# Kernel optimization log

Measured on AMD Instinct MI355X. Metric: run time of the kernel, lower is better.

Reference implementation:

```python
import jax, jax.numpy as jnp
import numpy as np

# Geometry constants (from init_kwargs)
H = 512            # volume rows
W = 512            # volume cols
N_ANGLES = 512     # number of projections
N_DET = 736        # detector bins (covers sqrt(2)*512 ~ 724 diagonal)
N_SAMP = 736       # integration samples along each ray
DET_SPACING = 1.0
STEP = 1.0         # ray sampling step (pixel units)


def _bilinear(img, px, py):
    """Bilinear interpolation of img[H,W] at float coords (px=col, py=row); zero outside."""
    x0 = jnp.floor(px)
    y0 = jnp.floor(py)
    fx = px - x0
    fy = py - y0
    x0i = x0.astype(jnp.int32)
    y0i = y0.astype(jnp.int32)

    def tap(yi, xi):
        valid = (xi >= 0) & (xi < W) & (yi >= 0) & (yi < H)
        v = img[jnp.clip(yi, 0, H - 1), jnp.clip(xi, 0, W - 1)]
        return jnp.where(valid, v, jnp.float32(0))

    v00 = tap(y0i, x0i)
    v01 = tap(y0i, x0i + 1)
    v10 = tap(y0i + 1, x0i)
    v11 = tap(y0i + 1, x0i + 1)
    return (v00 * (1 - fx) + v01 * fx) * (1 - fy) + (v10 * (1 - fx) + v11 * fx) * fy


def _parallel_projection2d(img, angles):
    """Parallel-beam Radon transform of img[H,W] -> sinogram [A, N_DET]."""
    cx = (W - 1) * 0.5
    cy = (H - 1) * 0.5
    # detector offsets s and ray-parameter samples t, centered
    s = (jnp.arange(N_DET, dtype=jnp.float32) - (N_DET - 1) * 0.5) * DET_SPACING
    t = (jnp.arange(N_SAMP, dtype=jnp.float32) - (N_SAMP - 1) * 0.5) * STEP

    def project_angle(theta):
        c = jnp.cos(theta)
        si = jnp.sin(theta)
        # ray point = s * (c, si) + t * (-si, c), shifted to image center. [D, T]
        px = s[:, None] * c - t[None, :] * si + cx
        py = s[:, None] * si + t[None, :] * c + cy
        return _bilinear(img, px, py).sum(axis=-1) * STEP  # [D]

    # sequential map over angles keeps intermediates at [D, T] instead of [A, D, T]
    return jax.lax.map(project_angle, angles)  # [A, D]


def setup_inputs() -> dict:
    key = jax.random.key(0)
    k1, k2 = jax.random.split(key)
    x = jax.random.normal(k1, (1, H, W), dtype=jnp.float32)
    # reco variable is constrained non-negative in the original (clip_by_value(x,0,inf))
    reco = jax.random.uniform(k2, (1, H, W), dtype=jnp.float32)
    angles = jnp.linspace(0.0, np.pi, N_ANGLES, endpoint=False, dtype=jnp.float32)
    return {"x": x, "reco": reco, "angles": angles}


def reference(x, reco, angles):
    updated_reco = x + reco                               # [1, H, W]
    sino = jax.vmap(lambda im: _parallel_projection2d(im, angles))(updated_reco)  # [1, A, D]
    return sino, reco
```

## Files before the change

kernel.cpp:

```cpp
#include <hip/hip_runtime.h>
#include <hip/hip_fp16.h>
#include <climits>


namespace {
constexpr int H = 512, W = 512, NA = 512, ND = 736, NS = 736;
constexpr int SINO_SIZE = NA * ND;
constexpr int IMG_SIZE = H * W;
constexpr int QN = 514;
constexpr int QS = 520;
constexpr int QUAD_SIZE = QN * QS;
constexpr int KSPLIT = 8;
}

typedef __fp16 h2 __attribute__((ext_vector_type(2)));
typedef float  f2 __attribute__((ext_vector_type(2)));

__global__ __launch_bounds__(256) void prep_quads(const float* __restrict__ x,
                                                  const float* __restrict__ reco,
                                                  uint2* __restrict__ Q,
                                                  uint2* __restrict__ QT,
                                                  float* __restrict__ reco_out,
                                                  float* __restrict__ sino) {
    __shared__ float tile[34][35];
    const int tx = threadIdx.x, ty = threadIdx.y;
    const int r0 = blockIdx.y * 32, c0 = blockIdx.x * 32;
    const int z  = blockIdx.z;

    if (z == 0) {
        const int nthr = 289 * 256;
        const int gtid = (blockIdx.y * 17 + blockIdx.x) * 256 + ty * 32 + tx;
        for (int i = gtid; i < SINO_SIZE; i += nthr) sino[i] = 0.f;
    }

    for (int li = ty * 32 + tx; li < 34 * 34; li += 256) {
        const int yy = li / 34, xx = li - yy * 34;
        const int r = r0 - 1 + yy, c = c0 - 1 + xx;
        float v = 0.f;
        if ((unsigned)r < 512u && (unsigned)c < 512u) {
            const int i = r * W + c;
            v = x[i] + reco[i];
        }
        tile[yy][xx] = v;
    }
    __syncthreads();

    const int t2 = ty + 8 * z;
    const int ri = r0 + t2, ci = c0 + tx;
    if (ri < QN && ci < QN) {
        uint2 q;
        q.x = __builtin_bit_cast(unsigned int,
              __builtin_amdgcn_cvt_pkrtz(tile[t2][tx],     tile[t2 + 1][tx]));
        q.y = __builtin_bit_cast(unsigned int,
              __builtin_amdgcn_cvt_pkrtz(tile[t2][tx + 1], tile[t2 + 1][tx + 1]));
        Q[ri * QS + ci] = q;
    }
    const int ri2 = c0 + t2, ci2 = r0 + tx;
    if (ri2 < QN && ci2 < QN) {
        uint2 q;
        q.x = __builtin_bit_cast(unsigned int,
              __builtin_amdgcn_cvt_pkrtz(tile[tx][t2],     tile[tx][t2 + 1]));
        q.y = __builtin_bit_cast(unsigned int,
              __builtin_amdgcn_cvt_pkrtz(tile[tx + 1][t2], tile[tx + 1][t2 + 1]));
        QT[ri2 * QS + ci2] = q;
    }
    const int rr = r0 + t2, cc = c0 + tx;
    if (rr < H && cc < W) reco_out[rr * W + cc] = reco[rr * W + cc];
}

__device__ inline void range1(float p0, float inc, float lo, float hi,
                              float& klo, float& khi) {
    if (inc > 1e-6f)       { klo = (lo - p0) / inc; khi = (hi - p0) / inc; }
    else if (inc < -1e-6f) { klo = (hi - p0) / inc; khi = (lo - p0) / inc; }
    else if (p0 >= lo && p0 <= hi) { klo = -1e9f; khi = 1e9f; }
    else                   { klo = 1e9f;  khi = -1e9f; }
}

__global__ __launch_bounds__(128) void proj_quad(const uint2* __restrict__ Q,
                                                 const uint2* __restrict__ QT,
                                                 const float* __restrict__ angles,
                                                 float* __restrict__ sino) {
    const int lane = threadIdx.x & 63;
    const int d = blockIdx.x * 128 + (threadIdx.x >> 6) * 64 + lane;
    const int a = blockIdx.y;
    const int z = blockIdx.z;

    float si, co;
    sincosf(angles[a], &si, &co);

    const float cx = (W - 1) * 0.5f, cy = (H - 1) * 0.5f;
    const float s  = (float)d - (ND - 1) * 0.5f;
    const float bx = fmaf(s, co, cx);
    const float by = fmaf(s, si, cy);

    const uint2* base;
    float f0, fi, s0, sl, dS;
    if (fabsf(co) >= fabsf(si)) { base = Q;  f0 = bx; fi = -si; s0 = by; sl = co;  dS = si; }
    else                        { base = QT; f0 = by; fi = co;  s0 = bx; sl = -si; dS = co; }

    const float t0 = -(float)(NS - 1) * 0.5f;
    float F0 = fmaf(t0, fi, f0);
    float S0 = fmaf(t0, sl, s0);
    if (sl < 0.f) {
        F0 = fmaf((float)(NS - 1), fi, F0); fi = -fi;
        S0 = fmaf((float)(NS - 1), sl, S0); sl = -sl;
    }

    float kloF, khiF, kloS, khiS;
    range1(F0, fi, -0.9999f, 511.9999f, kloF, khiF);
    range1(S0, sl, -0.9999f, 511.9999f, kloS, khiS);
    const int kA = max(0,      (int)ceilf(fmaxf(kloF, kloS)));
    const int kB = min(NS - 1, (int)floorf(fminf(khiF, khiS)));

    const int o = (int)rintf(-(float)lane * dS / sl);
    const float F1 = fmaf((float)o, fi, F0) + 1.f;
    const float S1 = fmaf((float)o, sl, S0) + 1.f;

    int jA, jB;
    if (kA <= kB) { jA = kA - o; jB = kB - o; }
    else          { jA = INT_MAX; jB = INT_MIN; }
    int Jlo = jA, Jhi = jB;
    #pragma unroll
    for (int off = 1; off < 64; off <<= 1) {
        Jlo = min(Jlo, __shfl_xor(Jlo, off));
        Jhi = max(Jhi, __shfl_xor(Jhi, off));
    }
    if (Jlo > Jhi) return;
    const int L  = Jhi - Jlo + 1;
    const int js = __builtin_amdgcn_readfirstlane(Jlo + (L * z) / KSPLIT);
    const int je = __builtin_amdgcn_readfirstlane(Jlo + (L * (z + 1)) / KSPLIT - 1);
    const int n  = je - js + 1;
    const int je2 = js + 2 * (n >> 1) - 1;

    const f2 fi2 = {fi, fi}, sl2 = {sl, sl};
    const f2 F12 = {F1, F1}, S12 = {S1, S1};
    f2 jf2 = {(float)js, (float)(js + 1)};
    float acc0 = 0.f, acc1 = 0.f;
    #pragma unroll 4
    for (int j = js; j <= je2; j += 2) {
        f2 pf = jf2 * fi2 + F12;
        f2 ps = jf2 * sl2 + S12;
        jf2 += (f2)2.f;
        pf = __builtin_elementwise_min(__builtin_elementwise_max(pf, (f2)0.f), (f2)513.f);
        ps = __builtin_elementwise_min(__builtin_elementwise_max(ps, (f2)0.f), (f2)513.f);
        const f2 ff = {__builtin_floorf(pf.x), __builtin_floorf(pf.y)};
        const f2 sf = {__builtin_floorf(ps.x), __builtin_floorf(ps.y)};
        const f2 fx = pf - ff;
        const f2 fy = ps - sf;
        const f2 gy = (f2)1.f - fy;
        const f2 aif = sf * (f2)520.f + ff;
        const unsigned a0 = (unsigned)aif.x;
        const unsigned a1 = (unsigned)aif.y;
        const uint2 q0 = base[a0];
        const uint2 q1 = base[a1];
        {
            const h2 l = __builtin_bit_cast(h2, q0.x);
            const h2 r = __builtin_bit_cast(h2, q0.y);
            const h2 fxx = __builtin_amdgcn_cvt_pkrtz(fx.x, fx.x);
            const h2 m = l + fxx * (r - l);
            const h2 wy = __builtin_amdgcn_cvt_pkrtz(gy.x, fy.x);
#if __has_builtin(__builtin_amdgcn_fdot2)
            acc0 = __builtin_amdgcn_fdot2(wy, m, acc0, false);
#else
            acc0 += (float)wy.x * (float)m.x + (float)wy.y * (float)m.y;
#endif
        }
        {
            const h2 l = __builtin_bit_cast(h2, q1.x);
            const h2 r = __builtin_bit_cast(h2, q1.y);
            const h2 fxx = __builtin_amdgcn_cvt_pkrtz(fx.y, fx.y);
            const h2 m = l + fxx * (r - l);
            const h2 wy = __builtin_amdgcn_cvt_pkrtz(gy.y, fy.y);
#if __has_builtin(__builtin_amdgcn_fdot2)
            acc1 = __builtin_amdgcn_fdot2(wy, m, acc1, false);
#else
            acc1 += (float)wy.x * (float)m.x + (float)wy.y * (float)m.y;
#endif
        }
    }
    if (n & 1) {
        const float jf = (float)je;
        float pf = fmaf(jf, fi, F1);
        float ps = fmaf(jf, sl, S1);
        pf = fminf(fmaxf(pf, 0.f), 513.f);
        ps = fminf(fmaxf(ps, 0.f), 513.f);
        const float ff = floorf(pf), sf = floorf(ps);
        const float fx = pf - ff,   fy = ps - sf;
        const unsigned ai = (unsigned)fmaf(sf, 520.f, ff);
        const uint2 q = base[ai];
        const h2 l = __builtin_bit_cast(h2, q.x);
        const h2 r = __builtin_bit_cast(h2, q.y);
        const h2 fxx = __builtin_amdgcn_cvt_pkrtz(fx, fx);
        const h2 m = l + fxx * (r - l);
        const h2 wy = __builtin_amdgcn_cvt_pkrtz(1.f - fy, fy);
#if __has_builtin(__builtin_amdgcn_fdot2)
        acc0 = __builtin_amdgcn_fdot2(wy, m, acc0, false);
#else
        acc0 += (float)wy.x * (float)m.x + (float)wy.y * (float)m.y;
#endif
    }
    const float acc = acc0 + acc1;
    if (d < ND)
        __hip_atomic_fetch_add(&sino[a * ND + d], acc,
                               __ATOMIC_RELAXED, __HIP_MEMORY_SCOPE_AGENT);
}

__global__ __launch_bounds__(256) void proj_fused(const float* __restrict__ A,
                                                  const float* __restrict__ B,
                                                  const float* __restrict__ angles,
                                                  float* __restrict__ sino) {
    const int d = blockIdx.x * blockDim.x + threadIdx.x;
    const int a = blockIdx.y;
    if (d >= ND) return;
    float si, c;
    sincosf(angles[a], &si, &c);
    const float cx = (W - 1) * 0.5f, cy = (H - 1) * 0.5f;
    const float s  = (float)d - (ND - 1) * 0.5f;
    const float bx = fmaf(s, c, cx), by = fmaf(s, si, cy);
    const float t0 = -(float)(NS - 1) * 0.5f;
    float acc = 0.f;
    for (int k = 0; k < NS; ++k) {
        const float t = t0 + (float)k;
        const float px = fmaf(t, -si, bx), py = fmaf(t, c, by);
        const float x0f = floorf(px), y0f = floorf(py);
        const float fx = px - x0f, fy = py - y0f;
        const int ix = (int)x0f, iy = (int)y0f;
        auto tap = [&](int yi, int xi) -> float {
            if (xi < 0 || xi >= W || yi < 0 || yi >= H) return 0.f;
            return A[yi * W + xi] + B[yi * W + xi];
        };
        float v = 0.f;
        if (ix >= -1 && iy >= -1 && ix <= W - 1 && iy <= H - 1) {
            const float v00 = tap(iy, ix),     v01 = tap(iy, ix + 1);
            const float v10 = tap(iy + 1, ix), v11 = tap(iy + 1, ix + 1);
            const float top = fmaf(fx, v01 - v00, v00);
            const float bot = fmaf(fx, v11 - v10, v10);
            v = fmaf(fy, bot - top, top);
        }
        acc += v;
    }
    sino[a * ND + d] = acc;
}

__global__ void prep_copy(const float* __restrict__ reco, float* __restrict__ reco_out) {
    int i = blockIdx.x * blockDim.x + threadIdx.x;
    if (i < IMG_SIZE) reco_out[i] = reco[i];
}

extern "C" void kernel_launch(void* const* d_in, const int* in_sizes, int n_in,
                              void* d_out, int out_size, void* d_ws, size_t ws_size,
                              hipStream_t stream) {
    const float* x      = (const float*)d_in[0];
    const float* reco   = (const float*)d_in[1];
    const float* angles = (const float*)d_in[2];
    float* sino     = (float*)d_out;
    float* reco_out = sino + SINO_SIZE;

    const size_t need_quads = 2 * (size_t)QUAD_SIZE * sizeof(uint2);

    if (ws_size >= need_quads) {
        uint2* Q  = (uint2*)d_ws;
        uint2* QT = Q + QUAD_SIZE;
        prep_quads<<<dim3(17, 17, 4), dim3(32, 8), 0, stream>>>(x, reco, Q, QT, reco_out, sino);
        proj_quad<<<dim3(6, NA, KSPLIT), dim3(128), 0, stream>>>(Q, QT, angles, sino);
    } else {
        prep_copy<<<dim3((IMG_SIZE + 255) / 256), dim3(256), 0, stream>>>(reco, reco_out);
        proj_fused<<<dim3((ND + 255) / 256, NA), dim3(256), 0, stream>>>(x, reco, angles, sino);
    }
}
```

Measured before the change: 147.7 us.

## Store horizontal deltas in quads and split loop into clamp-free interior

The precomputed fp16 quads now hold the left value and the right-minus-left difference, so the interpolation becomes one packed fma instead of a subtract plus an fma. The sample loop is split into a wave-uniform interior range, where every lane's sample is known to be in bounds, plus scalar clamped prologue and epilogue loops. Inside the interior the per-sample min/max clamping is dropped, and the two fx conversions are packed into a single cvt. In exchange the kernel does an extra range computation and reduction, and storing differences in fp16 changes rounding slightly.

Measured after the change: 160.8 us. +8.8%, slower.

```diff
diff --git a/kernel.cpp b/kernel.cpp
--- a/kernel.cpp
+++ b/kernel.cpp
@@ -52,7 +52,8 @@
         q.x = __builtin_bit_cast(unsigned int,
               __builtin_amdgcn_cvt_pkrtz(tile[t2][tx],     tile[t2 + 1][tx]));
         q.y = __builtin_bit_cast(unsigned int,
-              __builtin_amdgcn_cvt_pkrtz(tile[t2][tx + 1], tile[t2 + 1][tx + 1]));
+              __builtin_amdgcn_cvt_pkrtz(tile[t2][tx + 1]     - tile[t2][tx],
+                                         tile[t2 + 1][tx + 1] - tile[t2 + 1][tx]));
         Q[ri * QS + ci] = q;
     }
     const int ri2 = c0 + t2, ci2 = r0 + tx;
@@ -61,7 +62,8 @@
         q.x = __builtin_bit_cast(unsigned int,
               __builtin_amdgcn_cvt_pkrtz(tile[tx][t2],     tile[tx][t2 + 1]));
         q.y = __builtin_bit_cast(unsigned int,
-              __builtin_amdgcn_cvt_pkrtz(tile[tx + 1][t2], tile[tx + 1][t2 + 1]));
+              __builtin_amdgcn_cvt_pkrtz(tile[tx + 1][t2]     - tile[tx][t2],
+                                         tile[tx + 1][t2 + 1] - tile[tx][t2 + 1]));
         QT[ri2 * QS + ci2] = q;
     }
     const int rr = r0 + t2, cc = c0 + tx;
@@ -74,6 +76,30 @@
     else if (inc < -1e-6f) { klo = (hi - p0) / inc; khi = (lo - p0) / inc; }
     else if (p0 >= lo && p0 <= hi) { klo = -1e9f; khi = 1e9f; }
     else                   { klo = 1e9f;  khi = -1e9f; }
+}
+
+__device__ __forceinline__ void samp_clamped(const uint2* __restrict__ base,
+                                             float F1, float S1, float fi, float sl,
+                                             int j, float& acc) {
+    const float jf = (float)j;
+    float pf = fmaf(jf, fi, F1);
+    float ps = fmaf(jf, sl, S1);
+    pf = fminf(fmaxf(pf, 0.f), 513.f);
+    ps = fminf(fmaxf(ps, 0.f), 513.f);
+    const float ff = floorf(pf), sf = floorf(ps);
+    const float fx = pf - ff,   fy = ps - sf;
+    const unsigned ai = (unsigned)fmaf(sf, 520.f, ff);
+    const uint2 q = base[ai];
+    const h2 l  = __builtin_bit_cast(h2, q.x);
+    const h2 dl = __builtin_bit_cast(h2, q.y);
+    const h2 fxx = __builtin_amdgcn_cvt_pkrtz(fx, fx);
+    const h2 m = fxx * dl + l;
+    const h2 wy = __builtin_amdgcn_cvt_pkrtz(1.f - fy, fy);
+#if __has_builtin(__builtin_amdgcn_fdot2)
+    acc = __builtin_amdgcn_fdot2(wy, m, acc, false);
+#else
+    acc += (float)wy.x * (float)m.x + (float)wy.y * (float)m.y;
+#endif
 }
 
 __global__ __launch_bounds__(128) void proj_quad(const uint2* __restrict__ Q,
@@ -112,93 +138,98 @@
     const int kA = max(0,      (int)ceilf(fmaxf(kloF, kloS)));
     const int kB = min(NS - 1, (int)floorf(fminf(khiF, khiS)));
 
+    float iloF, ihiF, iloS, ihiS;
+    range1(F0, fi, -0.999f, 511.999f, iloF, ihiF);
+    range1(S0, sl, -0.999f, 511.999f, iloS, ihiS);
+    const int kAI = max(0,      (int)ceilf(fmaxf(iloF, iloS)));
+    const int kBI = min(NS - 1, (int)floorf(fminf(ihiF, ihiS)));
+
     const int o = (int)rintf(-(float)lane * dS / sl);
     const float F1 = fmaf((float)o, fi, F0) + 1.f;
     const float S1 = fmaf((float)o, sl, S0) + 1.f;
 
-    int jA, jB;
+    int jA, jB, iA, iB;
     if (kA <= kB) { jA = kA - o; jB = kB - o; }
     else          { jA = INT_MAX; jB = INT_MIN; }
-    int Jlo = jA, Jhi = jB;
+    if (kA <= kB && kAI <= kBI) { iA = kAI - o; iB = kBI - o; }
+    else                        { iA = INT_MAX; iB = INT_MIN; }
+
+    int Jlo = jA, Jhi = jB, Ilo = iA, Ihi = iB;
     #pragma unroll
     for (int off = 1; off < 64; off <<= 1) {
         Jlo = min(Jlo, __shfl_xor(Jlo, off));
         Jhi = max(Jhi, __shfl_xor(Jhi, off));
+        Ilo = max(Ilo, __shfl_xor(Ilo, off));
+        Ihi = min(Ihi, __shfl_xor(Ihi, off));
     }
     if (Jlo > Jhi) return;
     const int L  = Jhi - Jlo + 1;
     const int js = __builtin_amdgcn_readfirstlane(Jlo + (L * z) / KSPLIT);
     const int je = __builtin_amdgcn_readfirstlane(Jlo + (L * (z + 1)) / KSPLIT - 1);
-    const int n  = je - js + 1;
-    const int je2 = js + 2 * (n >> 1) - 1;
-
-    const f2 fi2 = {fi, fi}, sl2 = {sl, sl};
-    const f2 F12 = {F1, F1}, S12 = {S1, S1};
-    f2 jf2 = {(float)js, (float)(js + 1)};
+    if (js > je) return;
+
+    const int IAw = __builtin_amdgcn_readfirstlane(Ilo);
+    const int IBw = __builtin_amdgcn_readfirstlane(Ihi);
+    const int isI = max(js, IAw);
+    const int ieI = min(je, IBw);
+    int p0, nP2;
+    if (isI <= ieI) { p0 = isI;    nP2 = (ieI - isI + 1) & ~1; }
+    else            { p0 = je + 1; nP2 = 0; }
+
     float acc0 = 0.f, acc1 = 0.f;
-    #pragma unroll 4
-    for (int j = js; j <= je2; j += 2) {
-        f2 pf = jf2 * fi2 + F12;
-        f2 ps = jf2 * sl2 + S12;
-        jf2 += (f2)2.f;
-        pf = __builtin_elementwise_min(__builtin_elementwise_max(pf, (f2)0.f), (f2)513.f);
-        ps = __builtin_elementwise_min(__builtin_elementwise_max(ps, (f2)0.f), (f2)513.f);
-        const f2 ff = {__builtin_floorf(pf.x), __builtin_floorf(pf.y)};
-        const f2 sf = {__builtin_floorf(ps.x), __builtin_floorf(ps.y)};
-        const f2 fx = pf - ff;
-        const f2 fy = ps - sf;
-        const f2 gy = (f2)1.f - fy;
-        const f2 aif = sf * (f2)520.f + ff;
-        const unsigned a0 = (unsigned)aif.x;
-        const unsigned a1 = (unsigned)aif.y;
-        const uint2 q0 = base[a0];
-        const uint2 q1 = base[a1];
-        {
-            const h2 l = __builtin_bit_cast(h2, q0.x);
-            const h2 r = __builtin_bit_cast(h2, q0.y);
-            const h2 fxx = __builtin_amdgcn_cvt_pkrtz(fx.x, fx.x);
-            const h2 m = l + fxx * (r - l);
-            const h2 wy = __builtin_amdgcn_cvt_pkrtz(gy.x, fy.x);
+
+    for (int j = js; j < p0; ++j) samp_clamped(base, F1, S1, fi, sl, j, acc0);
+
+    if (nP2 > 0) {
+        const f2 fiv = {fi, fi}, slv = {sl, sl};
+        const f2 F1v = {F1, F1}, S1v = {S1, S1};
+        const f2 c520 = {520.f, 520.f};
+        f2 jf2 = {(float)p0, (float)(p0 + 1)};
+        #pragma unroll 4
+        for (int j = p0; j < p0 + nP2; j += 2) {
+            f2 pf = jf2 * fiv + F1v;
+            f2 ps = jf2 * slv + S1v;
+            jf2 += (f2)2.f;
+            const f2 ff = {__builtin_floorf(pf.x), __builtin_floorf(pf.y)};
+            const f2 sf = {__builtin_floorf(ps.x), __builtin_floorf(ps.y)};
+            const f2 fx = pf - ff;
+            const f2 fy = ps - sf;
+            const f2 gy = (f2)1.f - fy;
+            const f2 aif = sf * c520 + ff;
+            const unsigned a0 = (unsigned)aif.x;
+            const unsigned a1 = (unsigned)aif.y;
+            const uint2 q0 = base[a0];
+            const uint2 q1 = base[a1];
+            const h2 fxh = __builtin_amdgcn_cvt_pkrtz(fx.x, fx.y);
+            {
+                const h2 l   = __builtin_bit_cast(h2, q0.x);
+                const h2 dl  = __builtin_bit_cast(h2, q0.y);
+                const h2 fxx = {fxh.x, fxh.x};
+                const h2 m   = fxx * dl + l;
+                const h2 wy  = __builtin_amdgcn_cvt_pkrtz(gy.x, fy.x);
 #if __has_builtin(__builtin_amdgcn_fdot2)
-            acc0 = __builtin_amdgcn_fdot2(wy, m, acc0, false);
+                acc0 = __builtin_amdgcn_fdot2(wy, m, acc0, false);
 #else
-            acc0 += (float)wy.x * (float)m.x + (float)wy.y * (float)m.y;
+                acc0 += (float)wy.x * (float)m.x + (float)wy.y * (float)m.y;
 #endif
+            }
+            {
+                const h2 l   = __builtin_bit_cast(h2, q1.x);
+                const h2 dl  = __builtin_bit_cast(h2, q1.y);
+                const h2 fxx = {fxh.y, fxh.y};
+                const h2 m   = fxx * dl + l;
+                const h2 wy  = __builtin_amdgcn_cvt_pkrtz(gy.y, fy.y);
+#if __has_builtin(__builtin_amdgcn_fdot2)
+                acc1 = __builtin_amdgcn_fdot2(wy, m, acc1, false);
+#else
+                acc1 += (float)wy.x * (float)m.x + (float)wy.y * (float)m.y;
+#endif
+            }
         }
-        {
-            const h2 l = __builtin_bit_cast(h2, q1.x);
-            const h2 r = __builtin_bit_cast(h2, q1.y);
-            const h2 fxx = __builtin_amdgcn_cvt_pkrtz(fx.y, fx.y);
-            const h2 m = l + fxx * (r - l);
-            const h2 wy = __builtin_amdgcn_cvt_pkrtz(gy.y, fy.y);
-#if __has_builtin(__builtin_amdgcn_fdot2)
-            acc1 = __builtin_amdgcn_fdot2(wy, m, acc1, false);
-#else
-            acc1 += (float)wy.x * (float)m.x + (float)wy.y * (float)m.y;
-#endif
-        }
-    }
-    if (n & 1) {
-        const float jf = (float)je;
-        float pf = fmaf(jf, fi, F1);
-        float ps = fmaf(jf, sl, S1);
-        pf = fminf(fmaxf(pf, 0.f), 513.f);
-        ps = fminf(fmaxf(ps, 0.f), 513.f);
-        const float ff = floorf(pf), sf = floorf(ps);
-        const float fx = pf - ff,   fy = ps - sf;
-        const unsigned ai = (unsigned)fmaf(sf, 520.f, ff);
-        const uint2 q = base[ai];
-        const h2 l = __builtin_bit_cast(h2, q.x);
-        const h2 r = __builtin_bit_cast(h2, q.y);
-        const h2 fxx = __builtin_amdgcn_cvt_pkrtz(fx, fx);
-        const h2 m = l + fxx * (r - l);
-        const h2 wy = __builtin_amdgcn_cvt_pkrtz(1.f - fy, fy);
-#if __has_builtin(__builtin_amdgcn_fdot2)
-        acc0 = __builtin_amdgcn_fdot2(wy, m, acc0, false);
-#else
-        acc0 += (float)wy.x * (float)m.x + (float)wy.y * (float)m.y;
-#endif
-    }
+    }
+
+    for (int j = p0 + nP2; j <= je; ++j) samp_clamped(base, F1, S1, fi, sl, j, acc1);
+
     const float acc = acc0 + acc1;
     if (d < ND)
         __hip_atomic_fetch_add(&sino[a * ND + d], acc,
```
